# Kernel tuning notes

Hardware: AMD Instinct MI355X
Metric: run time of the kernel (lower is better)

## Reference

```python
import jax, jax.numpy as jnp
import numpy as np
from jax import lax

PATCH_SIZE = 7
NEIGH_SIZE = 9
SIGMA = 2.0
EPS = 1e-05


def _gaussian_kernel(sigma, sz):
    mid = sz // 2
    ax = np.arange(sz) - mid
    g = np.exp(-(ax[:, None] ** 2 + ax[None, :] ** 2) / (2.0 * sigma ** 2)) / (2.0 * np.pi * sigma ** 2)
    return g.astype(np.float32)


KERNEL = jnp.asarray(_gaussian_kernel(SIGMA, PATCH_SIZE))[None, None]  # (1,1,7,7)

_half = NEIGH_SIZE // 2
SHIFTS = jnp.asarray(
    [(x, y) for x in range(-_half, NEIGH_SIZE - _half)
     for y in range(-_half, NEIGH_SIZE - _half) if (x, y) != (0, 0)],
    dtype=jnp.int32)  # (80, 2) — xshift outer loop, yshift inner, matching torch order
SHIFTS4 = jnp.asarray([(-1, 0), (1, 0), (0, -1), (0, 1)], dtype=jnp.int32)


def _translate(img, tx, ty):
    # Faithful to torch affine_grid + grid_sample(nearest, zeros, align_corners=False):
    # a 'translation' of tx in normalized coords samples input at pixel j + tx*W/2.
    # H, W even and tx, ty integers -> exact integer pixel shifts, zero padding.
    H, W = img.shape
    px = jnp.arange(W) + tx * (W // 2)
    py = jnp.arange(H) + ty * (H // 2)
    mask = ((py >= 0) & (py < H))[:, None] & ((px >= 0) & (px < W))[None, :]
    out = img[jnp.clip(py, 0, H - 1)[:, None], jnp.clip(px, 0, W - 1)[None, :]]
    return jnp.where(mask, out, jnp.zeros((), img.dtype))


def _blur(x):
    # x: (N, H, W); conv2d with gaussian kernel, stride 1, padding 3 (same for 7x7)
    y = lax.conv_general_dilated(x[:, None], KERNEL, (1, 1), [(3, 3), (3, 3)],
                                 dimension_numbers=('NCHW', 'OIHW', 'NCHW'))
    return y[:, 0]


def _dp_batch(img2d, shifts):
    # Dp for a batch of shifts: shift, diff, square, gaussian blur
    shifted = jax.vmap(lambda s: _translate(img2d, s[0], s[1]))(shifts)  # (N,H,W)
    return _blur((img2d[None] - shifted) ** 2)


def setup_inputs() -> dict:
    key = jax.random.key(0)
    k1, k2 = jax.random.split(key)
    image1 = jax.random.normal(k1, (1, 1, 1024, 1024), dtype=jnp.float32)
    image2 = jax.random.normal(k2, (1, 1, 1024, 1024), dtype=jnp.float32)
    return {"image1": image1, "image2": image2}


def reference(image1, image2):
    img1 = image1[0, 0]  # (H, W)
    img2 = image2[0, 0]
    H, W = img1.shape
    reduce_size = (PATCH_SIZE + NEIGH_SIZE - 2) // 2  # = 7
    # Vimg: average of 4 single-pixel-neighborhood Dp's on image1, + eps
    Vimg = _dp_batch(img1, SHIFTS4).sum(axis=0) / 4.0 + EPS  # (H, W)
    # 80-shift MIND responses on image2
    D2 = _dp_batch(img2, SHIFTS)  # (80, H, W)
    mind = jnp.exp(-D2 / Vimg[None])
    # torch slices: dim1 end index is (C - reduce_size) = 1-7 = -6 -> H-6;
    # dim2 end index is (H - reduce_size). Replicated exactly (H == W).
    out = mind[:, reduce_size:H + 1 - reduce_size, reduce_size:H - reduce_size]
    mx = jnp.max(out, axis=0)
    return jnp.mean(out / mx[None])
```

## Files before the change

### kernel.cpp

```cpp
#include <hip/hip_runtime.h>
#include <cmath>

#define IMG_W 1024
#define SROWS 22
#define SCOLS 70

struct GK { float gh[7]; float gv[7]; };

__global__ __launch_bounds__(256)
void mind_tile(const float* __restrict__ img1, const float* __restrict__ img2,
               float* __restrict__ out, GK gk)
{
    __shared__ float4 s1[SROWS * SCOLS];

    const int tx  = (int)threadIdx.x;
    const int ty  = (int)threadIdx.y;
    const int tid = ty * 64 + tx;
    const int x0  = 7 + 64 * (int)blockIdx.x;
    const int y0  = 7 + 16 * (int)blockIdx.y;

    #pragma unroll
    for (int k = 0; k < 7; ++k) {
        const int e = tid + 256 * k;
        if (e < SROWS * SCOLS) {
            const int r  = e / SCOLS;
            const int c  = e - r * SCOLS;
            const int sr = min(y0 - 3 + r, 1023);
            const int sc = min(x0 - 3 + c, 1023);
            const int srp = sr ^ 512;
            const int scp = sc ^ 512;
            const float a  = img2[sr  * IMG_W + sc ];
            const float b  = img2[sr  * IMG_W + scp];
            const float cc = img2[srp * IMG_W + sc ];
            const float d  = img2[srp * IMG_W + scp];
            const float u  = img1[sr  * IMG_W + sc ];
            const float ub = img1[sr  * IMG_W + scp];
            const float uc = img1[srp * IMG_W + sc ];
            const float a2 = a * a;
            const float tb = a - b, tc = a - cc, td = a - d;
            const float su = u - ub, sv = u - uc;
            float4 f;
            f.x = fmaf(tb, tb, -a2);
            f.y = fmaf(tc, tc, -a2);
            f.z = fmaf(td, td, -a2);
            f.w = fmaf(u, u + u, fmaf(su, su, sv * sv));
            s1[e] = f;
        }
    }
    __syncthreads();

    float glx[7], ghx[7];
    #pragma unroll
    for (int kx = 0; kx < 7; ++kx) {
        const bool lo = (((x0 - 3 + tx + kx) & 512) == 0);
        glx[kx] = lo ? gk.gh[kx] : 0.f;
        ghx[kx] = lo ? 0.f : gk.gh[kx];
    }

    float Ph[4]  = {0,0,0,0}, Qh[4]  = {0,0,0,0}, Pv[4] = {0,0,0,0}, Qv[4] = {0,0,0,0};
    float Ppp[4] = {0,0,0,0}, Ppm[4] = {0,0,0,0}, Pmp[4] = {0,0,0,0}, Pmm[4] = {0,0,0,0};
    float V4[4]  = {0,0,0,0};

    #pragma unroll
    for (int r = 0; r < 10; ++r) {
        const float4* __restrict__ row = &s1[(4 * ty + r) * SCOLS + tx];
        float hHlo = 0, hHhi = 0, hV = 0, hDlo = 0, hDhi = 0, hU = 0;
        #pragma unroll
        for (int kx = 0; kx < 7; ++kx) {
            const float4 g = row[kx];
            hHlo = fmaf(glx[kx],   g.x, hHlo);
            hHhi = fmaf(ghx[kx],   g.x, hHhi);
            hV   = fmaf(gk.gh[kx], g.y, hV);
            hDlo = fmaf(glx[kx],   g.z, hDlo);
            hDhi = fmaf(ghx[kx],   g.z, hDhi);
            hU   = fmaf(gk.gh[kx], g.w, hU);
        }
        const bool ylo = (((y0 + 4 * ty - 3 + r) & 512) == 0);
        #pragma unroll
        for (int o = 0; o < 4; ++o) {
            if (r - o >= 0 && r - o <= 6) {
                const float g  = gk.gv[r - o];
                const float wl = ylo ? g : 0.f;
                const float wh = ylo ? 0.f : g;
                Ph [o] = fmaf(g,  hHlo, Ph [o]);
                Qh [o] = fmaf(g,  hHhi, Qh [o]);
                Pv [o] = fmaf(wl, hV,   Pv [o]);
                Qv [o] = fmaf(wh, hV,   Qv [o]);
                Ppp[o] = fmaf(wl, hDlo, Ppp[o]);
                Ppm[o] = fmaf(wh, hDlo, Ppm[o]);
                Pmp[o] = fmaf(wl, hDhi, Pmp[o]);
                Pmm[o] = fmaf(wh, hDhi, Pmm[o]);
                V4 [o] = fmaf(g,  hU,   V4 [o]);
            }
        }
    }

    const bool xok = (x0 + tx <= 1016);
    float tsum = 0.f;
    #pragma unroll
    for (int o = 0; o < 4; ++o) {
        const float V = fmaf(V4[o], 0.25f, 1e-5f);
        const float invV = 1.0f / V;
        float M = fminf(0.f, Ph[o]);
        M = fminf(M, Qh[o]);  M = fminf(M, Pv[o]);  M = fminf(M, Qv[o]);
        M = fminf(M, Ppp[o]); M = fminf(M, Pmp[o]); M = fminf(M, Ppm[o]); M = fminf(M, Pmm[o]);
        const float pix = 72.f * __expf(M * invV)
            + __expf((M - Ph [o]) * invV) + __expf((M - Qh [o]) * invV)
            + __expf((M - Pv [o]) * invV) + __expf((M - Qv [o]) * invV)
            + __expf((M - Ppp[o]) * invV) + __expf((M - Pmp[o]) * invV)
            + __expf((M - Ppm[o]) * invV) + __expf((M - Pmm[o]) * invV);
        const bool ok = xok && (y0 + 4 * ty + o <= 1017);
        tsum += ok ? pix : 0.f;
    }

    #pragma unroll
    for (int off = 32; off > 0; off >>= 1)
        tsum += __shfl_down(tsum, off, 64);
    __shared__ float wsum[4];
    if (tx == 0) wsum[ty] = tsum;
    __syncthreads();
    if (tid == 0) {
        const float bt = wsum[0] + wsum[1] + wsum[2] + wsum[3];
        atomicAdd(out, bt * (1.0f / 81688800.0f));
    }
}

extern "C" void kernel_launch(void* const* d_in, const int* in_sizes, int n_in,
                              void* d_out, int out_size, void* d_ws, size_t ws_size,
                              hipStream_t stream) {
    const float* img1 = (const float*)d_in[0];
    const float* img2 = (const float*)d_in[1];
    float* out = (float*)d_out;

    GK gk;
    for (int i = 0; i < 7; ++i) {
        const double d = i - 3;
        gk.gh[i] = (float)std::exp(-(d * d) / 8.0);
        gk.gv[i] = (float)(std::exp(-(d * d) / 8.0) / (8.0 * M_PI));
    }

    hipMemsetAsync(d_out, 0, sizeof(float), stream);
    dim3 block(64, 4);
    dim3 grid(16, 64);
    mind_tile<<<grid, block, 0, stream>>>(img1, img2, out, gk);
}
```

Baseline: 79.43 us.

## Add fast path for tiles away from half-image seams, two-stage reduction

Tiles whose stencil footprint does not cross the x=512 or y=512 seam take a simplified path. There each shift class collapses to a single blurred response, so the path uses 4 accumulators instead of 9 and computes 4 exponentials per pixel instead of 9. Seam-crossing tiles keep the original general path. The global atomicAdd plus memset is replaced by per-block partials written to workspace and a second single-block reduce kernel. This adds a kernel launch and some code-size and branch cost.

Measured after the change: 70.77 us. 1.12x faster.

```diff
diff --git a/kernel.cpp b/kernel.cpp
--- a/kernel.cpp
+++ b/kernel.cpp
@@ -7,9 +7,18 @@
 
 struct GK { float gh[7]; float gv[7]; };
 
+__device__ __forceinline__ float warp_block_sum(float v, float* wsum, int tx, int ty) {
+    #pragma unroll
+    for (int off = 32; off > 0; off >>= 1)
+        v += __shfl_down(v, off, 64);
+    if (tx == 0) wsum[ty] = v;
+    __syncthreads();
+    return wsum[0] + wsum[1] + wsum[2] + wsum[3];
+}
+
 __global__ __launch_bounds__(256)
 void mind_tile(const float* __restrict__ img1, const float* __restrict__ img2,
-               float* __restrict__ out, GK gk)
+               float* __restrict__ partials, GK gk)
 {
     __shared__ float4 s1[SROWS * SCOLS];
 
@@ -49,80 +58,136 @@
     }
     __syncthreads();
 
-    float glx[7], ghx[7];
-    #pragma unroll
-    for (int kx = 0; kx < 7; ++kx) {
-        const bool lo = (((x0 - 3 + tx + kx) & 512) == 0);
-        glx[kx] = lo ? gk.gh[kx] : 0.f;
-        ghx[kx] = lo ? 0.f : gk.gh[kx];
-    }
-
-    float Ph[4]  = {0,0,0,0}, Qh[4]  = {0,0,0,0}, Pv[4] = {0,0,0,0}, Qv[4] = {0,0,0,0};
-    float Ppp[4] = {0,0,0,0}, Ppm[4] = {0,0,0,0}, Pmp[4] = {0,0,0,0}, Pmm[4] = {0,0,0,0};
-    float V4[4]  = {0,0,0,0};
-
-    #pragma unroll
-    for (int r = 0; r < 10; ++r) {
-        const float4* __restrict__ row = &s1[(4 * ty + r) * SCOLS + tx];
-        float hHlo = 0, hHhi = 0, hV = 0, hDlo = 0, hDhi = 0, hU = 0;
-        #pragma unroll
-        for (int kx = 0; kx < 7; ++kx) {
-            const float4 g = row[kx];
-            hHlo = fmaf(glx[kx],   g.x, hHlo);
-            hHhi = fmaf(ghx[kx],   g.x, hHhi);
-            hV   = fmaf(gk.gh[kx], g.y, hV);
-            hDlo = fmaf(glx[kx],   g.z, hDlo);
-            hDhi = fmaf(ghx[kx],   g.z, hDhi);
-            hU   = fmaf(gk.gh[kx], g.w, hU);
-        }
-        const bool ylo = (((y0 + 4 * ty - 3 + r) & 512) == 0);
-        #pragma unroll
-        for (int o = 0; o < 4; ++o) {
-            if (r - o >= 0 && r - o <= 6) {
-                const float g  = gk.gv[r - o];
-                const float wl = ylo ? g : 0.f;
-                const float wh = ylo ? 0.f : g;
-                Ph [o] = fmaf(g,  hHlo, Ph [o]);
-                Qh [o] = fmaf(g,  hHhi, Qh [o]);
-                Pv [o] = fmaf(wl, hV,   Pv [o]);
-                Qv [o] = fmaf(wh, hV,   Qv [o]);
-                Ppp[o] = fmaf(wl, hDlo, Ppp[o]);
-                Ppm[o] = fmaf(wh, hDlo, Ppm[o]);
-                Pmp[o] = fmaf(wl, hDhi, Pmp[o]);
-                Pmm[o] = fmaf(wh, hDhi, Pmm[o]);
-                V4 [o] = fmaf(g,  hU,   V4 [o]);
-            }
-        }
-    }
-
+    const bool xs = (x0 - 3 <= 511) && (x0 + 66 >= 512);
+    const bool ys = (y0 - 3 <= 511) && (y0 + 18 >= 512);
     const bool xok = (x0 + tx <= 1016);
     float tsum = 0.f;
-    #pragma unroll
-    for (int o = 0; o < 4; ++o) {
-        const float V = fmaf(V4[o], 0.25f, 1e-5f);
-        const float invV = 1.0f / V;
-        float M = fminf(0.f, Ph[o]);
-        M = fminf(M, Qh[o]);  M = fminf(M, Pv[o]);  M = fminf(M, Qv[o]);
-        M = fminf(M, Ppp[o]); M = fminf(M, Pmp[o]); M = fminf(M, Ppm[o]); M = fminf(M, Pmm[o]);
-        const float pix = 72.f * __expf(M * invV)
-            + __expf((M - Ph [o]) * invV) + __expf((M - Qh [o]) * invV)
-            + __expf((M - Pv [o]) * invV) + __expf((M - Qv [o]) * invV)
-            + __expf((M - Ppp[o]) * invV) + __expf((M - Pmp[o]) * invV)
-            + __expf((M - Ppm[o]) * invV) + __expf((M - Pmm[o]) * invV);
-        const bool ok = xok && (y0 + 4 * ty + o <= 1017);
-        tsum += ok ? pix : 0.f;
+
+    if (!xs && !ys) {
+        const bool xlo = ((x0 & 512) == 0);
+        const bool ylo = ((y0 & 512) == 0);
+        float Px[4] = {0,0,0,0}, Py[4] = {0,0,0,0}, Pd[4] = {0,0,0,0}, V4[4] = {0,0,0,0};
+        #pragma unroll
+        for (int r = 0; r < 10; ++r) {
+            const float4* __restrict__ row = &s1[(4 * ty + r) * SCOLS + tx];
+            float hH = 0, hV = 0, hD = 0, hU = 0;
+            #pragma unroll
+            for (int kx = 0; kx < 7; ++kx) {
+                const float4 g = row[kx];
+                hH = fmaf(gk.gh[kx], g.x, hH);
+                hV = fmaf(gk.gh[kx], g.y, hV);
+                hD = fmaf(gk.gh[kx], g.z, hD);
+                hU = fmaf(gk.gh[kx], g.w, hU);
+            }
+            #pragma unroll
+            for (int o = 0; o < 4; ++o) {
+                if (r - o >= 0 && r - o <= 6) {
+                    const float g = gk.gv[r - o];
+                    Px[o] = fmaf(g, hH, Px[o]);
+                    Py[o] = fmaf(g, hV, Py[o]);
+                    Pd[o] = fmaf(g, hD, Pd[o]);
+                    V4[o] = fmaf(g, hU, V4[o]);
+                }
+            }
+        }
+        (void)xlo; (void)ylo;
+        #pragma unroll
+        for (int o = 0; o < 4; ++o) {
+            const float V = fmaf(V4[o], 0.25f, 1e-5f);
+            const float invV = 1.0f / V;
+            float M = fminf(0.f, Px[o]);
+            M = fminf(M, Py[o]); M = fminf(M, Pd[o]);
+            const float pix = 77.f * __expf(M * invV)
+                + __expf((M - Px[o]) * invV)
+                + __expf((M - Py[o]) * invV)
+                + __expf((M - Pd[o]) * invV);
+            const bool ok = xok && (y0 + 4 * ty + o <= 1017);
+            tsum += ok ? pix : 0.f;
+        }
+    } else {
+        float glx[7], ghx[7];
+        #pragma unroll
+        for (int kx = 0; kx < 7; ++kx) {
+            const bool lo = (((x0 - 3 + tx + kx) & 512) == 0);
+            glx[kx] = lo ? gk.gh[kx] : 0.f;
+            ghx[kx] = lo ? 0.f : gk.gh[kx];
+        }
+        float Ph[4]  = {0,0,0,0}, Qh[4]  = {0,0,0,0}, Pv[4] = {0,0,0,0}, Qv[4] = {0,0,0,0};
+        float Ppp[4] = {0,0,0,0}, Ppm[4] = {0,0,0,0}, Pmp[4] = {0,0,0,0}, Pmm[4] = {0,0,0,0};
+        float V4[4]  = {0,0,0,0};
+        #pragma unroll
+        for (int r = 0; r < 10; ++r) {
+            const float4* __restrict__ row = &s1[(4 * ty + r) * SCOLS + tx];
+            float hHlo = 0, hHhi = 0, hV = 0, hDlo = 0, hDhi = 0, hU = 0;
+            #pragma unroll
+            for (int kx = 0; kx < 7; ++kx) {
+                const float4 g = row[kx];
+                hHlo = fmaf(glx[kx],   g.x, hHlo);
+                hHhi = fmaf(ghx[kx],   g.x, hHhi);
+                hV   = fmaf(gk.gh[kx], g.y, hV);
+                hDlo = fmaf(glx[kx],   g.z, hDlo);
+                hDhi = fmaf(ghx[kx],   g.z, hDhi);
+                hU   = fmaf(gk.gh[kx], g.w, hU);
+            }
+            const bool ylo = (((y0 + 4 * ty - 3 + r) & 512) == 0);
+            #pragma unroll
+            for (int o = 0; o < 4; ++o) {
+                if (r - o >= 0 && r - o <= 6) {
+                    const float g  = gk.gv[r - o];
+                    const float wl = ylo ? g : 0.f;
+                    const float wh = ylo ? 0.f : g;
+                    Ph [o] = fmaf(g,  hHlo, Ph [o]);
+                    Qh [o] = fmaf(g,  hHhi, Qh [o]);
+                    Pv [o] = fmaf(wl, hV,   Pv [o]);
+                    Qv [o] = fmaf(wh, hV,   Qv [o]);
+                    Ppp[o] = fmaf(wl, hDlo, Ppp[o]);
+                    Ppm[o] = fmaf(wh, hDlo, Ppm[o]);
+                    Pmp[o] = fmaf(wl, hDhi, Pmp[o]);
+                    Pmm[o] = fmaf(wh, hDhi, Pmm[o]);
+                    V4 [o] = fmaf(g,  hU,   V4 [o]);
+                }
+            }
+        }
+        #pragma unroll
+        for (int o = 0; o < 4; ++o) {
+            const float V = fmaf(V4[o], 0.25f, 1e-5f);
+            const float invV = 1.0f / V;
+            float M = fminf(0.f, Ph[o]);
+            M = fminf(M, Qh[o]);  M = fminf(M, Pv[o]);  M = fminf(M, Qv[o]);
+            M = fminf(M, Ppp[o]); M = fminf(M, Pmp[o]); M = fminf(M, Ppm[o]); M = fminf(M, Pmm[o]);
+            const float pix = 72.f * __expf(M * invV)
+                + __expf((M - Ph [o]) * invV) + __expf((M - Qh [o]) * invV)
+                + __expf((M - Pv [o]) * invV) + __expf((M - Qv [o]) * invV)
+                + __expf((M - Ppp[o]) * invV) + __expf((M - Pmp[o]) * invV)
+                + __expf((M - Ppm[o]) * invV) + __expf((M - Pmm[o]) * invV);
+            const bool ok = xok && (y0 + 4 * ty + o <= 1017);
+            tsum += ok ? pix : 0.f;
+        }
     }
 
+    __shared__ float wsum[4];
+    const float bt = warp_block_sum(tsum, wsum, tx, ty);
+    if (tid == 0)
+        partials[(int)blockIdx.y * gridDim.x + (int)blockIdx.x] = bt;
+}
+
+__global__ __launch_bounds__(256)
+void mind_reduce(const float* __restrict__ partials, float* __restrict__ out)
+{
+    float s = 0.f;
+    #pragma unroll
+    for (int k = 0; k < 4; ++k)
+        s += partials[(int)threadIdx.x + 256 * k];
+    double d = (double)s;
     #pragma unroll
     for (int off = 32; off > 0; off >>= 1)
-        tsum += __shfl_down(tsum, off, 64);
-    __shared__ float wsum[4];
-    if (tx == 0) wsum[ty] = tsum;
+        d += __shfl_down(d, off, 64);
+    __shared__ double sm[4];
+    const int lane = (int)threadIdx.x & 63, wid = (int)threadIdx.x >> 6;
+    if (lane == 0) sm[wid] = d;
     __syncthreads();
-    if (tid == 0) {
-        const float bt = wsum[0] + wsum[1] + wsum[2] + wsum[3];
-        atomicAdd(out, bt * (1.0f / 81688800.0f));
-    }
+    if (threadIdx.x == 0)
+        out[0] = (float)((sm[0] + sm[1] + sm[2] + sm[3]) / 81688800.0);
 }
 
 extern "C" void kernel_launch(void* const* d_in, const int* in_sizes, int n_in,
@@ -131,6 +196,7 @@
     const float* img1 = (const float*)d_in[0];
     const float* img2 = (const float*)d_in[1];
     float* out = (float*)d_out;
+    float* partials = (float*)d_ws;
 
     GK gk;
     for (int i = 0; i < 7; ++i) {
@@ -139,8 +205,8 @@
         gk.gv[i] = (float)(std::exp(-(d * d) / 8.0) / (8.0 * M_PI));
     }
 
-    hipMemsetAsync(d_out, 0, sizeof(float), stream);
     dim3 block(64, 4);
     dim3 grid(16, 64);
-    mind_tile<<<grid, block, 0, stream>>>(img1, img2, out, gk);
-}
+    mind_tile<<<grid, block, 0, stream>>>(img1, img2, partials, gk);
+    mind_reduce<<<1, 256, 0, stream>>>(partials, out);
+}
```
